# Kernel tuning notes

Hardware: AMD Instinct MI355X
Metric: run time of the kernel (lower is better)

## Reference

```python
import jax, jax.numpy as jnp
import numpy as np

B, N, D, E, A, DIAM = 16, 1024, 128, 16384, 64, 3


def setup_inputs() -> dict:
    key = jax.random.key(0)
    ks = jax.random.split(key, 20)
    s = 0.05
    inp = {
        "node_features": jax.random.normal(ks[0], (B, N, D), jnp.float32),
        "edge_features": jax.random.normal(ks[1], (B, N, N), jnp.float32),
        "src_idx": jax.random.randint(ks[2], (E,), 0, N, jnp.int32),
        "tgt_idx": jax.random.randint(ks[3], (E,), 0, N, jnp.int32),
        # message MLP: Linear(2D+1 -> D)
        "W_msg": jax.random.normal(ks[4], (2 * D + 1, D), jnp.float32) * s,
        "b_msg": jax.random.normal(ks[5], (D,), jnp.float32) * s,
        # GRUCell(D, D), gate order r,z,n (torch convention)
        "W_ih": jax.random.normal(ks[6], (3 * D, D), jnp.float32) * s,
        "W_hh": jax.random.normal(ks[7], (3 * D, D), jnp.float32) * s,
        "b_ih": jax.random.normal(ks[8], (3 * D,), jnp.float32) * s,
        "b_hh": jax.random.normal(ks[9], (3 * D,), jnp.float32) * s,
        # readout: Linear(D,D)+SELU, Linear(D,D)+SELU, then policy head Linear(D,A)
        "W_r1": jax.random.normal(ks[10], (D, D), jnp.float32) * s,
        "b_r1": jax.random.normal(ks[11], (D,), jnp.float32) * s,
        "W_r2": jax.random.normal(ks[12], (D, D), jnp.float32) * s,
        "b_r2": jax.random.normal(ks[13], (D,), jnp.float32) * s,
        "W_pol": jax.random.normal(ks[14], (D, A), jnp.float32) * s,
        "b_pol": jax.random.normal(ks[15], (A,), jnp.float32) * s,
    }
    return inp


def reference(node_features, edge_features, src_idx, tgt_idx,
              W_msg, b_msg, W_ih, W_hh, b_ih, b_hh,
              W_r1, b_r1, W_r2, b_r2, W_pol, b_pol):
    h = node_features  # [B, N, D]
    ef = edge_features[:, src_idx, tgt_idx][..., None]  # [B, E, 1], constant across rounds
    for _ in range(DIAM):
        src_f = h[:, src_idx]  # [B, E, D] gather
        tgt_f = h[:, tgt_idx]  # [B, E, D]
        comb = jnp.concatenate([src_f, tgt_f, ef], axis=-1)  # [B, E, 2D+1]
        msg = jax.nn.selu(comb @ W_msg + b_msg)  # [B, E, D]
        # scatter-sum messages onto target nodes
        agg = jax.vmap(lambda m: jax.ops.segment_sum(m, tgt_idx, num_segments=N))(msg)  # [B, N, D]
        # GRUCell update (torch math, gate order r,z,n; b_hn stays inside r*(...))
        gi = agg @ W_ih.T + b_ih  # [B, N, 3D]
        gh = h @ W_hh.T + b_hh    # [B, N, 3D]
        i_r, i_z, i_n = jnp.split(gi, 3, axis=-1)
        h_r, h_z, h_n = jnp.split(gh, 3, axis=-1)
        r = jax.nn.sigmoid(i_r + h_r)
        z = jax.nn.sigmoid(i_z + h_z)
        n = jnp.tanh(i_n + r * h_n)
        h = (1.0 - z) * n + z * h
    pooled = h.sum(axis=1)  # [B, D]
    pooled = jax.nn.selu(pooled @ W_r1 + b_r1)
    pooled = jax.nn.selu(pooled @ W_r2 + b_r2)
    return pooled @ W_pol + b_pol  # [B, A] policy logits
```

## Files before the change

### kernel.cpp

```cpp
#include <hip/hip_runtime.h>
#include <hip/hip_bf16.h>
#include <math.h>

constexpr int kB = 16;
constexpr int kN = 1024;
constexpr int kD = 128;
constexpr int kE = 16384;

typedef short bf16x8 __attribute__((ext_vector_type(8)));
typedef float f32x4 __attribute__((ext_vector_type(4)));
typedef unsigned short us4 __attribute__((ext_vector_type(4)));

__device__ __forceinline__ float selu_f(float x) {
    const float scale = 1.0507009873554805f;
    const float alpha = 1.6732632423543772f;
    return x > 0.f ? scale * x : scale * alpha * (expf(x) - 1.f);
}

__device__ __forceinline__ float sigmoid_f(float x) {
    return 1.f / (1.f + expf(-x));
}

__device__ __forceinline__ float bf2f(unsigned short u) {
    union { unsigned int i; float f; } x;
    x.i = ((unsigned int)u) << 16;
    return x.f;
}

__device__ __forceinline__ unsigned short f2bf(float f) {
    union { float f; unsigned int i; } u;
    u.f = f;
    const unsigned int r = u.i + 0x7fffu + ((u.i >> 16) & 1u);
    return (unsigned short)(r >> 16);
}

__global__ void k_h0c(const float* __restrict__ nodef, unsigned short* __restrict__ h_bf,
                      const int* __restrict__ tgt, int* __restrict__ cnt) {
    int gid = blockIdx.x * 256 + threadIdx.x;
    h_bf[gid] = f2bf(nodef[gid]);
    if (gid < kE) atomicAdd(&cnt[tgt[gid]], 1);
}

__global__ void k_scan(const int* __restrict__ cnt, int* __restrict__ cursor,
                       int* __restrict__ rowstart) {
    __shared__ int s[kN];
    int t = threadIdx.x;
    int own = cnt[t];
    s[t] = own;
    __syncthreads();
    for (int off = 1; off < kN; off <<= 1) {
        int add = (t >= off) ? s[t - off] : 0;
        __syncthreads();
        s[t] += add;
        __syncthreads();
    }
    int excl = s[t] - own;
    cursor[t] = excl;
    rowstart[t] = excl;
    if (t == kN - 1) rowstart[kN] = s[t];
}

__global__ void k_scatter(const int* __restrict__ src, const int* __restrict__ tgt,
                          int* __restrict__ cursor, int* __restrict__ sid,
                          int* __restrict__ ssrc) {
    int e = blockIdx.x * 256 + threadIdx.x;
    int tg = tgt[e];
    int pos = atomicAdd(&cursor[tg], 1);
    sid[pos] = e;
    ssrc[pos] = src[e];
}

__global__ void k_gather_ef(const float* __restrict__ edgef, const int* __restrict__ src,
                            const int* __restrict__ tgt, const int* __restrict__ sid,
                            float* __restrict__ efg) {
    int gid = blockIdx.x * 256 + threadIdx.x;
    int b = gid >> 14;
    int i = gid & (kE - 1);
    int eid = sid[i];
    efg[gid] = edgef[(size_t)b * kN * kN + (size_t)src[eid] * kN + tgt[eid]];
}

__global__ void k_buildw(const float* __restrict__ Wmsg, const float* __restrict__ Whh,
                         const float* __restrict__ Wih,
                         const float* __restrict__ bih, const float* __restrict__ bhh,
                         unsigned short* __restrict__ WcatT,
                         unsigned short* __restrict__ Wfused,
                         float* __restrict__ bihP, float* __restrict__ bhhP) {
    const int j = blockIdx.x;
    const int k = threadIdx.x;
    if (j < 256) {
        float v = (j < 128) ? Wmsg[k * 128 + j] : Wmsg[(128 + k) * 128 + (j - 128)];
        WcatT[j * 128 + k] = f2bf(v);
    } else {
        const int f = j - 256;
        const int dg = f / 48, rem = f % 48;
        const int g = rem / 16, di = rem % 16;
        const int orig = g * 128 + dg * 16 + di;
        Wfused[(size_t)f * 256 + k] = f2bf(Wih[(size_t)orig * 128 + k]);
        Wfused[(size_t)f * 256 + 128 + k] = f2bf(Whh[(size_t)orig * 128 + k]);
        if (k == 0) {
            bihP[f] = bih[orig];
            bhhP[f] = bhh[orig];
        }
    }
}

__launch_bounds__(256)
__global__ void k_mm256(const unsigned short* __restrict__ A,
                        const unsigned short* __restrict__ Bt,
                        unsigned short* __restrict__ HST) {
    __shared__ uint4 As[2048];
    __shared__ uint4 Bs[2048];
    const int t = threadIdx.x;
    const int r0 = blockIdx.x * 128;
    const int c0 = blockIdx.y * 128;
    const uint4* gA = (const uint4*)(A + (size_t)r0 * 128);
    const uint4* gB = (const uint4*)(Bt + (size_t)c0 * 128);
#pragma unroll
    for (int i = 0; i < 8; ++i) {
        const int f = i * 256 + t;
        const int row = f >> 4, c16 = f & 15;
        const int d = row * 16 + (c16 ^ (row & 7));
        As[d] = gA[f];
        Bs[d] = gB[f];
    }
    __syncthreads();
    const int w = t >> 6, l = t & 63;
    const int wm = (w & 1) * 64, wn = (w >> 1) * 64;
    const int lin = l & 15, kq = l >> 4;
    f32x4 acc[4][4] = {};
#pragma unroll
    for (int s = 0; s < 4; ++s) {
        bf16x8 a[4], b[4];
#pragma unroll
        for (int mi = 0; mi < 4; ++mi) {
            const int row = wm + mi * 16 + lin;
            a[mi] = *(const bf16x8*)&As[row * 16 + ((s * 4 + kq) ^ (row & 7))];
        }
#pragma unroll
        for (int ni = 0; ni < 4; ++ni) {
            const int row = wn + ni * 16 + lin;
            b[ni] = *(const bf16x8*)&Bs[row * 16 + ((s * 4 + kq) ^ (row & 7))];
        }
#pragma unroll
        for (int mi = 0; mi < 4; ++mi)
#pragma unroll
            for (int ni = 0; ni < 4; ++ni)
                acc[mi][ni] = __builtin_amdgcn_mfma_f32_16x16x32_bf16(
                    a[mi], b[ni], acc[mi][ni], 0, 0, 0);
    }
    const int rq = kq * 4;
#pragma unroll
    for (int ni = 0; ni < 4; ++ni) {
        const int col = c0 + wn + ni * 16 + lin;
#pragma unroll
        for (int mi = 0; mi < 4; ++mi) {
            const int row = r0 + wm + mi * 16 + rq;
#pragma unroll
            for (int r = 0; r < 4; ++r)
                HST[(size_t)(row + r) * 256 + col] = f2bf(acc[mi][ni][r]);
        }
    }
}

__launch_bounds__(256)
__global__ void k_edge(const unsigned short* __restrict__ HST, const float* __restrict__ efg,
                       const int* __restrict__ ssrc, const int* __restrict__ rowstart,
                       const float* __restrict__ Wmsg, const float* __restrict__ bmsg,
                       unsigned short* __restrict__ agg_bf) {
    __shared__ float4 part[2][4][32];
    const int t = threadIdx.x;
    const int b = blockIdx.y;
    const int tl = t >> 7;
    const int tg = blockIdx.x * 2 + tl;
    const int slot = (t >> 5) & 3;
    const int lane = t & 31;
    const int c = lane * 4;
    const float4 w3 = *(const float4*)&Wmsg[256 * 128 + c];
    const float4 bm = *(const float4*)&bmsg[c];
    const size_t base = (size_t)b * kN;
    const us4 htu = *(const us4*)&HST[(base + tg) * 256 + 128 + c];
    const float hb0 = bf2f(htu.x) + bm.x;
    const float hb1 = bf2f(htu.y) + bm.y;
    const float hb2 = bf2f(htu.z) + bm.z;
    const float hb3 = bf2f(htu.w) + bm.w;
    const float* efb = efg + b * kE;
    const int j0 = rowstart[tg], j1 = rowstart[tg + 1];
    float a0 = 0.f, a1 = 0.f, a2 = 0.f, a3 = 0.f;
    for (int j = j0 + slot; j < j1; j += 4) {
        const int s = ssrc[j];
        const float ef = efb[j];
        const us4 hs = *(const us4*)&HST[(base + s) * 256 + c];
        a0 += selu_f(bf2f(hs.x) + fmaf(ef, w3.x, hb0));
        a1 += selu_f(bf2f(hs.y) + fmaf(ef, w3.y, hb1));
        a2 += selu_f(bf2f(hs.z) + fmaf(ef, w3.z, hb2));
        a3 += selu_f(bf2f(hs.w) + fmaf(ef, w3.w, hb3));
    }
    part[tl][slot][lane] = make_float4(a0, a1, a2, a3);
    __syncthreads();
    if (slot == 0) {
        const float4 p1 = part[tl][1][lane];
        const float4 p2 = part[tl][2][lane];
        const float4 p3 = part[tl][3][lane];
        a0 += p1.x + p2.x + p3.x;
        a1 += p1.y + p2.y + p3.y;
        a2 += p1.z + p2.z + p3.z;
        a3 += p1.w + p2.w + p3.w;
        us4 o;
        o.x = f2bf(a0);
        o.y = f2bf(a1);
        o.z = f2bf(a2);
        o.w = f2bf(a3);
        *(us4*)&agg_bf[(base + tg) * 128 + c] = o;
    }
}

__launch_bounds__(256)
__global__ void k_gigru(const unsigned short* __restrict__ agg_bf,
                        const unsigned short* __restrict__ h_bf_in,
                        const unsigned short* __restrict__ Wfused,
                        const float* __restrict__ bihP, const float* __restrict__ bhhP,
                        unsigned short* __restrict__ h_bf_out,
                        float* __restrict__ pooled, int lastIter) {
    __shared__ uint4 As[2048];
    __shared__ uint4 Bs[1536];
    const int t = threadIdx.x;
    const int r0 = blockIdx.x * 128;
    const int y = blockIdx.y;
    const int w = t >> 6, l = t & 63;
    const int wm = (w & 1) * 64, wc0 = (w >> 1) * 48;
    const int lin = l & 15, kq = l >> 4, rq = kq * 4;
    f32x4 acc[4][3] = {};
    f32x4 accN[4] = {};
#pragma unroll
    for (int stage = 0; stage < 2; ++stage) {
        const unsigned short* Ap = stage ? h_bf_in : agg_bf;
        const uint4* gA = (const uint4*)(Ap + (size_t)r0 * 128);
#pragma unroll
        for (int i = 0; i < 8; ++i) {
            const int f = i * 256 + t;
            const int row = f >> 4, c16 = f & 15;
            As[row * 16 + (c16 ^ (row & 7))] = gA[f];
        }
        const uint4* gW = (const uint4*)Wfused;
#pragma unroll
        for (int i = 0; i < 6; ++i) {
            const int f = i * 256 + t;
            const int j = f >> 4, c16 = f & 15;
            Bs[j * 16 + (c16 ^ (j & 7))] = gW[(size_t)(y * 96 + j) * 32 + stage * 16 + c16];
        }
        __syncthreads();
#pragma unroll
        for (int ks = 0; ks < 4; ++ks) {
            bf16x8 a[4], b[3];
#pragma unroll
            for (int mi = 0; mi < 4; ++mi) {
                const int row = wm + mi * 16 + lin;
                a[mi] = *(const bf16x8*)&As[row * 16 + ((ks * 4 + kq) ^ (row & 7))];
            }
#pragma unroll
            for (int ni = 0; ni < 3; ++ni) {
                const int row = wc0 + ni * 16 + lin;
                b[ni] = *(const bf16x8*)&Bs[row * 16 + ((ks * 4 + kq) ^ (row & 7))];
            }
#pragma unroll
            for (int mi = 0; mi < 4; ++mi) {
                acc[mi][0] = __builtin_amdgcn_mfma_f32_16x16x32_bf16(a[mi], b[0], acc[mi][0], 0, 0, 0);
                acc[mi][1] = __builtin_amdgcn_mfma_f32_16x16x32_bf16(a[mi], b[1], acc[mi][1], 0, 0, 0);
                if (stage == 0)
                    acc[mi][2] = __builtin_amdgcn_mfma_f32_16x16x32_bf16(a[mi], b[2], acc[mi][2], 0, 0, 0);
                else
                    accN[mi] = __builtin_amdgcn_mfma_f32_16x16x32_bf16(a[mi], b[2], accN[mi], 0, 0, 0);
            }
        }
        __syncthreads();
    }
    const int colR = y * 96 + wc0 + lin;
    const float bR = bihP[colR] + bhhP[colR];
    const float bZ = bihP[colR + 16] + bhhP[colR + 16];
    const float biN = bihP[colR + 32];
    const float bhN = bhhP[colR + 32];
    const int dgg = y * 2 + (wc0 / 48);
    const int d = dgg * 16 + lin;
    const int bb = r0 >> 10;
    const int dc = d >> 3, de = d & 7;
    float psum = 0.f;
#pragma unroll
    for (int mi = 0; mi < 4; ++mi) {
#pragma unroll
        for (int r = 0; r < 4; ++r) {
            const int rowL = wm + mi * 16 + rq + r;
            const float rr = sigmoid_f(acc[mi][0][r] + bR);
            const float zz = sigmoid_f(acc[mi][1][r] + bZ);
            const float i_n = acc[mi][2][r] + biN;
            const float h_n = accN[mi][r] + bhN;
            const float nn = tanhf(fmaf(rr, h_n, i_n));
            const float hv = bf2f(((const unsigned short*)&As[rowL * 16 + (dc ^ (rowL & 7))])[de]);
            const float o = fmaf(zz, hv - nn, nn);
            h_bf_out[(size_t)(r0 + rowL) * 128 + d] = f2bf(o);
            psum += o;
        }
    }
    if (lastIter) atomicAdd(&pooled[bb * 128 + d], psum);
}

__global__ void k_head(const float* __restrict__ pooled,
                       const float* __restrict__ Wr1, const float* __restrict__ br1,
                       const float* __restrict__ Wr2, const float* __restrict__ br2,
                       const float* __restrict__ Wpol, const float* __restrict__ bpol,
                       float* __restrict__ out) {
    __shared__ float p[128], t1[128];
    const int b = blockIdx.x, d = threadIdx.x;
    p[d] = pooled[b * 128 + d];
    __syncthreads();
    float acc = br1[d];
    for (int k = 0; k < 128; ++k) acc = fmaf(p[k], Wr1[k * 128 + d], acc);
    t1[d] = selu_f(acc);
    __syncthreads();
    acc = br2[d];
    for (int k = 0; k < 128; ++k) acc = fmaf(t1[k], Wr2[k * 128 + d], acc);
    __syncthreads();
    p[d] = selu_f(acc);
    __syncthreads();
    if (d < 64) {
        float o = bpol[d];
        for (int k = 0; k < 128; ++k) o = fmaf(p[k], Wpol[k * 64 + d], o);
        out[b * 64 + d] = o;
    }
}

extern "C" void kernel_launch(void* const* d_in, const int* in_sizes, int n_in,
                              void* d_out, int out_size, void* d_ws, size_t ws_size,
                              hipStream_t stream) {
    const float* nodef = (const float*)d_in[0];
    const float* edgef = (const float*)d_in[1];
    const int* src = (const int*)d_in[2];
    const int* tgt = (const int*)d_in[3];
    const float* Wmsg = (const float*)d_in[4];
    const float* bmsg = (const float*)d_in[5];
    const float* Wih = (const float*)d_in[6];
    const float* Whh = (const float*)d_in[7];
    const float* bih = (const float*)d_in[8];
    const float* bhh = (const float*)d_in[9];
    const float* Wr1 = (const float*)d_in[10];
    const float* br1 = (const float*)d_in[11];
    const float* Wr2 = (const float*)d_in[12];
    const float* br2 = (const float*)d_in[13];
    const float* Wpol = (const float*)d_in[14];
    const float* bpol = (const float*)d_in[15];
    float* out = (float*)d_out;

    float* ws = (float*)d_ws;
    float* efg = ws;
    float* bihP = efg + 262144;
    float* bhhP = bihP + 384;
    int* cnt = (int*)(bhhP + 384);
    float* pooled = (float*)(cnt + 1024);
    unsigned short* HST = (unsigned short*)(pooled + 2048);
    unsigned short* hbfA = HST + 4194304;
    unsigned short* hbfB = hbfA + 2097152;
    unsigned short* agg_bf = hbfB + 2097152;
    unsigned short* WcatT = agg_bf + 2097152;
    unsigned short* Wfused = WcatT + 32768;
    int* cursor = (int*)(Wfused + 98304);
    int* rowstart = cursor + 1024;
    int* sid = rowstart + 1040;
    int* ssrc = sid + 16384;

    hipMemsetAsync(cnt, 0, (1024 + 2048) * sizeof(int), stream);
    k_h0c<<<(kB * kN * kD) / 256, 256, 0, stream>>>(nodef, hbfA, tgt, cnt);
    k_scan<<<1, 1024, 0, stream>>>(cnt, cursor, rowstart);
    k_scatter<<<kE / 256, 256, 0, stream>>>(src, tgt, cursor, sid, ssrc);
    k_gather_ef<<<(kB * kE) / 256, 256, 0, stream>>>(edgef, src, tgt, sid, efg);
    k_buildw<<<640, 128, 0, stream>>>(Wmsg, Whh, Wih, bih, bhh, WcatT, Wfused, bihP, bhhP);

    for (int it = 0; it < 3; ++it) {
        unsigned short* hcur = (it & 1) ? hbfB : hbfA;
        unsigned short* hnxt = (it & 1) ? hbfA : hbfB;
        k_mm256<<<dim3(128, 2), 256, 0, stream>>>(hcur, WcatT, HST);
        k_edge<<<dim3(kN / 2, kB), 256, 0, stream>>>(HST, efg, ssrc, rowstart, Wmsg, bmsg, agg_bf);
        k_gigru<<<dim3(128, 4), 256, 0, stream>>>(agg_bf, hcur, Wfused, bihP, bhhP, hnxt,
                                                  pooled, it == 2 ? 1 : 0);
    }

    k_head<<<kB, 128, 0, stream>>>(pooled, Wr1, br1, Wr2, br2, Wpol, bpol, out);
}
```

Baseline: 299.5 us.

## Fuse whole pipeline into one cooperative persistent kernel with grid syncs

Replaces the sequence of about fifteen separate launches (setup, scan, scatter, gather, weight build, three rounds of matmul/edge/GRU, head) with a single cooperative kernel of 256 blocks that separates the phases with grid.sync(). The aim is to remove per-launch overhead and inter-kernel gaps. In exchange, every phase is limited to 256 blocks with 64KB of shared memory each, so the edge and GRU phases have lower occupancy and parallelism. Each grid barrier also has its own cost. The multi-kernel path remains as a fallback when cooperative launch is unavailable.

```diff
diff --git a/kernel.cpp b/kernel.cpp
--- a/kernel.cpp
+++ b/kernel.cpp
@@ -1,6 +1,8 @@
 #include <hip/hip_runtime.h>
-#include <hip/hip_bf16.h>
+#include <hip/hip_cooperative_groups.h>
 #include <math.h>
+
+namespace cg = cooperative_groups;
 
 constexpr int kB = 16;
 constexpr int kN = 1024;
@@ -32,6 +34,321 @@
     u.f = f;
     const unsigned int r = u.i + 0x7fffu + ((u.i >> 16) & 1u);
     return (unsigned short)(r >> 16);
+}
+
+struct MParams {
+    const float* nodef; const float* edgef; const int* src; const int* tgt;
+    const float* Wmsg; const float* bmsg; const float* Wih; const float* Whh;
+    const float* bih; const float* bhh;
+    const float* Wr1; const float* br1; const float* Wr2; const float* br2;
+    const float* Wpol; const float* bpol;
+    float* out;
+    float* efg; float* bihP; float* bhhP; int* cnt; float* pooled;
+    unsigned short* HST; unsigned short* hbfA; unsigned short* hbfB;
+    unsigned short* agg; unsigned short* WcatT; unsigned short* Wfused;
+    int* cursor; int* rowstart; int* sid; int* ssrc;
+};
+
+__launch_bounds__(256)
+__global__ void k_mega(MParams P) {
+    cg::grid_group grid = cg::this_grid();
+    __shared__ __align__(16) unsigned char smemraw[65536];
+    uint4* smem = (uint4*)smemraw;
+    const int blk = blockIdx.x;
+    const int t = threadIdx.x;
+
+    {
+#pragma unroll
+        for (int i = 0; i < 8; ++i) {
+            const int base = blk * 8192 + i * 1024 + t * 4;
+            const float4 v = *(const float4*)&P.nodef[base];
+            us4 o;
+            o.x = f2bf(v.x); o.y = f2bf(v.y); o.z = f2bf(v.z); o.w = f2bf(v.w);
+            *(us4*)&P.hbfA[base] = o;
+        }
+        if (blk == 254) for (int i = t; i < 1024; i += 256) P.cnt[i] = 0;
+        if (blk == 255) for (int i = t; i < 2048; i += 256) P.pooled[i] = 0.f;
+    }
+    grid.sync();
+    if (blk < 64) atomicAdd(&P.cnt[P.tgt[blk * 256 + t]], 1);
+    grid.sync();
+    if (blk == 0) {
+        int* wsum = (int*)smemraw;
+        const int t4 = t * 4;
+        const int v0 = P.cnt[t4], v1 = P.cnt[t4 + 1], v2 = P.cnt[t4 + 2], v3 = P.cnt[t4 + 3];
+        wsum[t] = v0 + v1 + v2 + v3;
+        __syncthreads();
+        for (int off = 1; off < 256; off <<= 1) {
+            const int add = (t >= off) ? wsum[t - off] : 0;
+            __syncthreads();
+            wsum[t] += add;
+            __syncthreads();
+        }
+        int run = t ? wsum[t - 1] : 0;
+        P.cursor[t4] = run; P.rowstart[t4] = run; run += v0;
+        P.cursor[t4 + 1] = run; P.rowstart[t4 + 1] = run; run += v1;
+        P.cursor[t4 + 2] = run; P.rowstart[t4 + 2] = run; run += v2;
+        P.cursor[t4 + 3] = run; P.rowstart[t4 + 3] = run; run += v3;
+        if (t == 255) P.rowstart[1024] = run;
+    } else if (blk <= 160) {
+#pragma unroll
+        for (int jj = 0; jj < 2; ++jj) {
+            const int j = (blk - 1) * 4 + jj * 2 + (t >> 7);
+            const int k = t & 127;
+            if (j < 256) {
+                float v = (j < 128) ? P.Wmsg[k * 128 + j] : P.Wmsg[(128 + k) * 128 + (j - 128)];
+                P.WcatT[j * 128 + k] = f2bf(v);
+            } else {
+                const int f = j - 256;
+                const int dg = f / 48, rem = f % 48;
+                const int g = rem / 16, di = rem % 16;
+                const int orig = g * 128 + dg * 16 + di;
+                P.Wfused[(size_t)f * 256 + k] = f2bf(P.Wih[(size_t)orig * 128 + k]);
+                P.Wfused[(size_t)f * 256 + 128 + k] = f2bf(P.Whh[(size_t)orig * 128 + k]);
+                if (k == 0) { P.bihP[f] = P.bih[orig]; P.bhhP[f] = P.bhh[orig]; }
+            }
+        }
+    }
+    grid.sync();
+    if (blk < 64) {
+        const int e = blk * 256 + t;
+        const int tg = P.tgt[e];
+        const int pos = atomicAdd(&P.cursor[tg], 1);
+        P.sid[pos] = e;
+        P.ssrc[pos] = P.src[e];
+    }
+    grid.sync();
+#pragma unroll
+    for (int i = 0; i < 4; ++i) {
+        const int gid = blk * 1024 + i * 256 + t;
+        const int b = gid >> 14, idx = gid & (kE - 1);
+        const int eid = P.sid[idx];
+        P.efg[gid] = P.edgef[((size_t)b << 20) + ((size_t)P.src[eid] << 10) + P.tgt[eid]];
+    }
+    grid.sync();
+
+    const int w = t >> 6, l = t & 63;
+    const int lin = l & 15, kq = l >> 4, rq = kq * 4;
+    for (int it = 0; it < 3; ++it) {
+        const unsigned short* hcur = (it & 1) ? P.hbfB : P.hbfA;
+        unsigned short* hnxt = (it & 1) ? P.hbfA : P.hbfB;
+
+        {
+            uint4* As = smem;
+            uint4* Bs = smem + 2048;
+            const int r0 = (blk & 127) * 128;
+            const int c0 = (blk >> 7) * 128;
+            const uint4* gA = (const uint4*)(hcur + (size_t)r0 * 128);
+            const uint4* gB = (const uint4*)(P.WcatT + (size_t)c0 * 128);
+#pragma unroll
+            for (int i = 0; i < 8; ++i) {
+                const int f = i * 256 + t;
+                const int row = f >> 4, c16 = f & 15;
+                const int d = row * 16 + (c16 ^ (row & 7));
+                As[d] = gA[f];
+                Bs[d] = gB[f];
+            }
+            __syncthreads();
+            const int wm = (w & 1) * 64, wn = (w >> 1) * 64;
+            f32x4 acc[4][4] = {};
+#pragma unroll
+            for (int s = 0; s < 4; ++s) {
+                bf16x8 a[4], b[4];
+#pragma unroll
+                for (int mi = 0; mi < 4; ++mi) {
+                    const int row = wm + mi * 16 + lin;
+                    a[mi] = *(const bf16x8*)&As[row * 16 + ((s * 4 + kq) ^ (row & 7))];
+                }
+#pragma unroll
+                for (int ni = 0; ni < 4; ++ni) {
+                    const int row = wn + ni * 16 + lin;
+                    b[ni] = *(const bf16x8*)&Bs[row * 16 + ((s * 4 + kq) ^ (row & 7))];
+                }
+#pragma unroll
+                for (int mi = 0; mi < 4; ++mi)
+#pragma unroll
+                    for (int ni = 0; ni < 4; ++ni)
+                        acc[mi][ni] = __builtin_amdgcn_mfma_f32_16x16x32_bf16(
+                            a[mi], b[ni], acc[mi][ni], 0, 0, 0);
+            }
+#pragma unroll
+            for (int ni = 0; ni < 4; ++ni) {
+                const int col = c0 + wn + ni * 16 + lin;
+#pragma unroll
+                for (int mi = 0; mi < 4; ++mi) {
+                    const int row = r0 + wm + mi * 16 + rq;
+#pragma unroll
+                    for (int r = 0; r < 4; ++r)
+                        P.HST[(size_t)(row + r) * 256 + col] = f2bf(acc[mi][ni][r]);
+                }
+            }
+            __syncthreads();
+        }
+        grid.sync();
+
+        {
+            float4* part = (float4*)smemraw;
+            const int tl = t >> 7;
+            const int slot = (t >> 5) & 3;
+            const int lane = t & 31;
+            const int c = lane * 4;
+            const float4 w3 = *(const float4*)&P.Wmsg[256 * 128 + c];
+            const float4 bm = *(const float4*)&P.bmsg[c];
+#pragma unroll 1
+            for (int u = 0; u < 32; ++u) {
+                const int unit = blk * 32 + u;
+                const int b = unit >> 9;
+                const int bx = unit & 511;
+                const int tg = bx * 2 + tl;
+                float4* pu = part + (u & 1) * 256;
+                const size_t base = (size_t)b * kN;
+                const us4 htu = *(const us4*)&P.HST[(base + tg) * 256 + 128 + c];
+                const float hb0 = bf2f(htu.x) + bm.x;
+                const float hb1 = bf2f(htu.y) + bm.y;
+                const float hb2 = bf2f(htu.z) + bm.z;
+                const float hb3 = bf2f(htu.w) + bm.w;
+                const float* efb = P.efg + b * kE;
+                const int j0 = P.rowstart[tg], j1 = P.rowstart[tg + 1];
+                float a0 = 0.f, a1 = 0.f, a2 = 0.f, a3 = 0.f;
+                for (int j = j0 + slot; j < j1; j += 4) {
+                    const int s = P.ssrc[j];
+                    const float ef = efb[j];
+                    const us4 hs = *(const us4*)&P.HST[(base + s) * 256 + c];
+                    a0 += selu_f(bf2f(hs.x) + fmaf(ef, w3.x, hb0));
+                    a1 += selu_f(bf2f(hs.y) + fmaf(ef, w3.y, hb1));
+                    a2 += selu_f(bf2f(hs.z) + fmaf(ef, w3.z, hb2));
+                    a3 += selu_f(bf2f(hs.w) + fmaf(ef, w3.w, hb3));
+                }
+                pu[(tl * 4 + slot) * 32 + lane] = make_float4(a0, a1, a2, a3);
+                __syncthreads();
+                if (slot == 0) {
+                    const float4 p1 = pu[(tl * 4 + 1) * 32 + lane];
+                    const float4 p2 = pu[(tl * 4 + 2) * 32 + lane];
+                    const float4 p3 = pu[(tl * 4 + 3) * 32 + lane];
+                    a0 += p1.x + p2.x + p3.x;
+                    a1 += p1.y + p2.y + p3.y;
+                    a2 += p1.z + p2.z + p3.z;
+                    a3 += p1.w + p2.w + p3.w;
+                    us4 o;
+                    o.x = f2bf(a0); o.y = f2bf(a1); o.z = f2bf(a2); o.w = f2bf(a3);
+                    *(us4*)&P.agg[(base + tg) * 128 + c] = o;
+                }
+            }
+            __syncthreads();
+        }
+        grid.sync();
+
+#pragma unroll 1
+        for (int sub = 0; sub < 2; ++sub) {
+            const int tile = blk + 256 * sub;
+            uint4* As = smem;
+            uint4* Bs = smem + 2048;
+            const int r0 = (tile & 127) * 128;
+            const int y = tile >> 7;
+            const int wm = (w & 1) * 64, wc0 = (w >> 1) * 48;
+            f32x4 acc[4][3] = {};
+            f32x4 accN[4] = {};
+#pragma unroll
+            for (int stage = 0; stage < 2; ++stage) {
+                const unsigned short* Ap = stage ? hcur : P.agg;
+                const uint4* gA = (const uint4*)(Ap + (size_t)r0 * 128);
+#pragma unroll
+                for (int i = 0; i < 8; ++i) {
+                    const int f = i * 256 + t;
+                    const int row = f >> 4, c16 = f & 15;
+                    As[row * 16 + (c16 ^ (row & 7))] = gA[f];
+                }
+                const uint4* gW = (const uint4*)P.Wfused;
+#pragma unroll
+                for (int i = 0; i < 6; ++i) {
+                    const int f = i * 256 + t;
+                    const int j = f >> 4, c16 = f & 15;
+                    Bs[j * 16 + (c16 ^ (j & 7))] = gW[(size_t)(y * 96 + j) * 32 + stage * 16 + c16];
+                }
+                __syncthreads();
+#pragma unroll
+                for (int ks = 0; ks < 4; ++ks) {
+                    bf16x8 a[4], b[3];
+#pragma unroll
+                    for (int mi = 0; mi < 4; ++mi) {
+                        const int row = wm + mi * 16 + lin;
+                        a[mi] = *(const bf16x8*)&As[row * 16 + ((ks * 4 + kq) ^ (row & 7))];
+                    }
+#pragma unroll
+                    for (int ni = 0; ni < 3; ++ni) {
+                        const int row = wc0 + ni * 16 + lin;
+                        b[ni] = *(const bf16x8*)&Bs[row * 16 + ((ks * 4 + kq) ^ (row & 7))];
+                    }
+#pragma unroll
+                    for (int mi = 0; mi < 4; ++mi) {
+                        acc[mi][0] = __builtin_amdgcn_mfma_f32_16x16x32_bf16(a[mi], b[0], acc[mi][0], 0, 0, 0);
+                        acc[mi][1] = __builtin_amdgcn_mfma_f32_16x16x32_bf16(a[mi], b[1], acc[mi][1], 0, 0, 0);
+                        if (stage == 0)
+                            acc[mi][2] = __builtin_amdgcn_mfma_f32_16x16x32_bf16(a[mi], b[2], acc[mi][2], 0, 0, 0);
+                        else
+                            accN[mi] = __builtin_amdgcn_mfma_f32_16x16x32_bf16(a[mi], b[2], accN[mi], 0, 0, 0);
+                    }
+                }
+                __syncthreads();
+            }
+            const int colR = y * 96 + wc0 + lin;
+            const float bR = P.bihP[colR] + P.bhhP[colR];
+            const float bZ = P.bihP[colR + 16] + P.bhhP[colR + 16];
+            const float biN = P.bihP[colR + 32];
+            const float bhN = P.bhhP[colR + 32];
+            const int dgg = y * 2 + (wc0 / 48);
+            const int d = dgg * 16 + lin;
+            const int bb = r0 >> 10;
+            const int dc = d >> 3, de = d & 7;
+            float psum = 0.f;
+#pragma unroll
+            for (int mi = 0; mi < 4; ++mi) {
+#pragma unroll
+                for (int r = 0; r < 4; ++r) {
+                    const int rowL = wm + mi * 16 + rq + r;
+                    const float rr = sigmoid_f(acc[mi][0][r] + bR);
+                    const float zz = sigmoid_f(acc[mi][1][r] + bZ);
+                    const float i_n = acc[mi][2][r] + biN;
+                    const float h_n = accN[mi][r] + bhN;
+                    const float nn = tanhf(fmaf(rr, h_n, i_n));
+                    const float hv = bf2f(((const unsigned short*)&As[rowL * 16 + (dc ^ (rowL & 7))])[de]);
+                    const float o = fmaf(zz, hv - nn, nn);
+                    hnxt[(size_t)(r0 + rowL) * 128 + d] = f2bf(o);
+                    psum += o;
+                }
+            }
+            if (it == 2) atomicAdd(&P.pooled[bb * 128 + d], psum);
+            __syncthreads();
+        }
+        grid.sync();
+    }
+
+    if (blk < 16) {
+        float* p = (float*)smemraw;
+        float* t1 = p + 128;
+        const int b = blk;
+        if (t < 128) p[t] = P.pooled[b * 128 + t];
+        __syncthreads();
+        if (t < 128) {
+            float acc = P.br1[t];
+            for (int k = 0; k < 128; ++k) acc = fmaf(p[k], P.Wr1[k * 128 + t], acc);
+            t1[t] = selu_f(acc);
+        }
+        __syncthreads();
+        float acc2 = 0.f;
+        if (t < 128) {
+            acc2 = P.br2[t];
+            for (int k = 0; k < 128; ++k) acc2 = fmaf(t1[k], P.Wr2[k * 128 + t], acc2);
+        }
+        __syncthreads();
+        if (t < 128) p[t] = selu_f(acc2);
+        __syncthreads();
+        if (t < 64) {
+            float o = P.bpol[t];
+            for (int k = 0; k < 128; ++k) o = fmaf(p[k], P.Wpol[k * 64 + t], o);
+            P.out[b * 64 + t] = o;
+        }
+    }
 }
 
 __global__ void k_h0c(const float* __restrict__ nodef, unsigned short* __restrict__ h_bf,
@@ -98,10 +415,7 @@
         const int orig = g * 128 + dg * 16 + di;
         Wfused[(size_t)f * 256 + k] = f2bf(Wih[(size_t)orig * 128 + k]);
         Wfused[(size_t)f * 256 + 128 + k] = f2bf(Whh[(size_t)orig * 128 + k]);
-        if (k == 0) {
-            bihP[f] = bih[orig];
-            bhhP[f] = bhh[orig];
-        }
+        if (k == 0) { bihP[f] = bih[orig]; bhhP[f] = bhh[orig]; }
     }
 }
 
@@ -207,10 +521,7 @@
         a2 += p1.z + p2.z + p3.z;
         a3 += p1.w + p2.w + p3.w;
         us4 o;
-        o.x = f2bf(a0);
-        o.y = f2bf(a1);
-        o.z = f2bf(a2);
-        o.w = f2bf(a3);
+        o.x = f2bf(a0); o.y = f2bf(a1); o.z = f2bf(a2); o.w = f2bf(a3);
         *(us4*)&agg_bf[(base + tg) * 128 + c] = o;
     }
 }
@@ -332,56 +643,73 @@
 extern "C" void kernel_launch(void* const* d_in, const int* in_sizes, int n_in,
                               void* d_out, int out_size, void* d_ws, size_t ws_size,
                               hipStream_t stream) {
-    const float* nodef = (const float*)d_in[0];
-    const float* edgef = (const float*)d_in[1];
-    const int* src = (const int*)d_in[2];
-    const int* tgt = (const int*)d_in[3];
-    const float* Wmsg = (const float*)d_in[4];
-    const float* bmsg = (const float*)d_in[5];
-    const float* Wih = (const float*)d_in[6];
-    const float* Whh = (const float*)d_in[7];
-    const float* bih = (const float*)d_in[8];
-    const float* bhh = (const float*)d_in[9];
-    const float* Wr1 = (const float*)d_in[10];
-    const float* br1 = (const float*)d_in[11];
-    const float* Wr2 = (const float*)d_in[12];
-    const float* br2 = (const float*)d_in[13];
-    const float* Wpol = (const float*)d_in[14];
-    const float* bpol = (const float*)d_in[15];
-    float* out = (float*)d_out;
+    MParams P;
+    P.nodef = (const float*)d_in[0];
+    P.edgef = (const float*)d_in[1];
+    P.src = (const int*)d_in[2];
+    P.tgt = (const int*)d_in[3];
+    P.Wmsg = (const float*)d_in[4];
+    P.bmsg = (const float*)d_in[5];
+    P.Wih = (const float*)d_in[6];
+    P.Whh = (const float*)d_in[7];
+    P.bih = (const float*)d_in[8];
+    P.bhh = (const float*)d_in[9];
+    P.Wr1 = (const float*)d_in[10];
+    P.br1 = (const float*)d_in[11];
+    P.Wr2 = (const float*)d_in[12];
+    P.br2 = (const float*)d_in[13];
+    P.Wpol = (const float*)d_in[14];
+    P.bpol = (const float*)d_in[15];
+    P.out = (float*)d_out;
 
     float* ws = (float*)d_ws;
-    float* efg = ws;
-    float* bihP = efg + 262144;
-    float* bhhP = bihP + 384;
-    int* cnt = (int*)(bhhP + 384);
-    float* pooled = (float*)(cnt + 1024);
-    unsigned short* HST = (unsigned short*)(pooled + 2048);
-    unsigned short* hbfA = HST + 4194304;
-    unsigned short* hbfB = hbfA + 2097152;
-    unsigned short* agg_bf = hbfB + 2097152;
-    unsigned short* WcatT = agg_bf + 2097152;
-    unsigned short* Wfused = WcatT + 32768;
-    int* cursor = (int*)(Wfused + 98304);
-    int* rowstart = cursor + 1024;
-    int* sid = rowstart + 1040;
-    int* ssrc = sid + 16384;
-
-    hipMemsetAsync(cnt, 0, (1024 + 2048) * sizeof(int), stream);
-    k_h0c<<<(kB * kN * kD) / 256, 256, 0, stream>>>(nodef, hbfA, tgt, cnt);
-    k_scan<<<1, 1024, 0, stream>>>(cnt, cursor, rowstart);
-    k_scatter<<<kE / 256, 256, 0, stream>>>(src, tgt, cursor, sid, ssrc);
-    k_gather_ef<<<(kB * kE) / 256, 256, 0, stream>>>(edgef, src, tgt, sid, efg);
-    k_buildw<<<640, 128, 0, stream>>>(Wmsg, Whh, Wih, bih, bhh, WcatT, Wfused, bihP, bhhP);
-
+    P.efg = ws;
+    P.bihP = P.efg + 262144;
+    P.bhhP = P.bihP + 384;
+    P.cnt = (int*)(P.bhhP + 384);
+    P.pooled = (float*)(P.cnt + 1024);
+    P.HST = (unsigned short*)(P.pooled + 2048);
+    P.hbfA = P.HST + 4194304;
+    P.hbfB = P.hbfA + 2097152;
+    P.agg = P.hbfB + 2097152;
+    P.WcatT = P.agg + 2097152;
+    P.Wfused = P.WcatT + 32768;
+    P.cursor = (int*)(P.Wfused + 98304);
+    P.rowstart = P.cursor + 1024;
+    P.sid = P.rowstart + 1040;
+    P.ssrc = P.sid + 16384;
+
+    int dev = 0;
+    hipGetDevice(&dev);
+    int coop = 0;
+    hipDeviceGetAttribute(&coop, hipDeviceAttributeCooperativeLaunch, dev);
+    int numCU = 0;
+    hipDeviceGetAttribute(&numCU, hipDeviceAttributeMultiprocessorCount, dev);
+    int maxBlk = 0;
+    hipOccupancyMaxActiveBlocksPerMultiprocessor(&maxBlk, k_mega, 256, 0);
+    const bool useCoop = coop && (maxBlk > 0) && ((long)maxBlk * numCU >= 256);
+
+    if (useCoop) {
+        void* args[] = {&P};
+        hipLaunchCooperativeKernel(k_mega, dim3(256), dim3(256), args, 0u, stream);
+        return;
+    }
+
+    hipMemsetAsync(P.cnt, 0, (1024 + 2048) * sizeof(int), stream);
+    k_h0c<<<(kB * kN * kD) / 256, 256, 0, stream>>>(P.nodef, P.hbfA, P.tgt, P.cnt);
+    k_scan<<<1, 1024, 0, stream>>>(P.cnt, P.cursor, P.rowstart);
+    k_scatter<<<kE / 256, 256, 0, stream>>>(P.src, P.tgt, P.cursor, P.sid, P.ssrc);
+    k_gather_ef<<<(kB * kE) / 256, 256, 0, stream>>>(P.edgef, P.src, P.tgt, P.sid, P.efg);
+    k_buildw<<<640, 128, 0, stream>>>(P.Wmsg, P.Whh, P.Wih, P.bih, P.bhh, P.WcatT, P.Wfused,
+                                      P.bihP, P.bhhP);
     for (int it = 0; it < 3; ++it) {
-        unsigned short* hcur = (it & 1) ? hbfB : hbfA;
-        unsigned short* hnxt = (it & 1) ? hbfA : hbfB;
-        k_mm256<<<dim3(128, 2), 256, 0, stream>>>(hcur, WcatT, HST);
-        k_edge<<<dim3(kN / 2, kB), 256, 0, stream>>>(HST, efg, ssrc, rowstart, Wmsg, bmsg, agg_bf);
-        k_gigru<<<dim3(128, 4), 256, 0, stream>>>(agg_bf, hcur, Wfused, bihP, bhhP, hnxt,
-                                                  pooled, it == 2 ? 1 : 0);
-    }
-
-    k_head<<<kB, 128, 0, stream>>>(pooled, Wr1, br1, Wr2, br2, Wpol, bpol, out);
-}
+        unsigned short* hcur = (it & 1) ? P.hbfB : P.hbfA;
+        unsigned short* hnxt = (it & 1) ? P.hbfA : P.hbfB;
+        k_mm256<<<dim3(128, 2), 256, 0, stream>>>(hcur, P.WcatT, P.HST);
+        k_edge<<<dim3(kN / 2, kB), 256, 0, stream>>>(P.HST, P.efg, P.ssrc, P.rowstart,
+                                                     P.Wmsg, P.bmsg, P.agg);
+        k_gigru<<<dim3(128, 4), 256, 0, stream>>>(P.agg, hcur, P.Wfused, P.bihP, P.bhhP, hnxt,
+                                                  P.pooled, it == 2 ? 1 : 0);
+    }
+    k_head<<<kB, 128, 0, stream>>>(P.pooled, P.Wr1, P.br1, P.Wr2, P.br2, P.Wpol, P.bpol, P.out);
+}
```

New measurement: 301.4 us. About the same (+0.6%).
